# Optimization experiments

Hardware: AMD Instinct MI355X
Metric: run time of the kernel (lower is better)

## Reference

```python
import jax, jax.numpy as jnp
import numpy as np

B, T1, T2, NFEAT, H = 8, 512, 1500, 1024, 16
DK = NFEAT // H


def setup_inputs() -> dict:
    key = jax.random.key(0)
    ks = jax.random.split(key, 8)
    s = 0.02
    return {
        "x": jax.random.normal(ks[0], (B, T1, NFEAT), dtype=jnp.float32),
        "memory": jax.random.normal(ks[1], (B, T2, NFEAT), dtype=jnp.float32),
        "memory_mask": jnp.ones((B, 1, T2), dtype=jnp.int32),
        "Wq": jax.random.normal(ks[2], (NFEAT, NFEAT), dtype=jnp.float32) * s,
        "bq": jnp.zeros((NFEAT,), dtype=jnp.float32),
        "Wkv": jax.random.normal(ks[3], (NFEAT, 2 * NFEAT), dtype=jnp.float32) * s,
        "bkv": jnp.zeros((2 * NFEAT,), dtype=jnp.float32),
        "Wout": jax.random.normal(ks[4], (NFEAT, NFEAT), dtype=jnp.float32) * s,
        "bout": jnp.zeros((NFEAT,), dtype=jnp.float32),
    }


def reference(x, memory, memory_mask, Wq, bq, Wkv, bkv, Wout, bout):
    b, t1, _ = x.shape
    t2 = memory.shape[1]
    # projections (W stored as (in, out))
    q = x @ Wq + bq                                   # (b, t1, n_feat)
    kv = memory @ Wkv + bkv                           # (b, t2, 2*n_feat)
    k, v = jnp.split(kv, 2, axis=-1)
    q_h = q.reshape(b, t1, H, DK).transpose(0, 2, 1, 3)   # (b,h,t1,dk)
    k_h = k.reshape(b, t2, H, DK).transpose(0, 2, 1, 3)   # (b,h,t2,dk)
    v_h = v.reshape(b, t2, H, DK).transpose(0, 2, 1, 3)   # (b,h,t2,dk)
    q_h = q_h * (DK ** -0.5)
    scores = jnp.einsum("bhqd,bhkd->bhqk", q_h, k_h)      # (b,h,t1,t2)
    mask0 = (memory_mask[:, None, :, :] == 0)             # (b,1,1 or t1,t2)
    scores = jnp.where(mask0, -jnp.inf, scores)
    attn = jax.nn.softmax(scores, axis=-1)
    attn = jnp.where(mask0, 0.0, attn)
    ctx = jnp.einsum("bhqk,bhkd->bhqd", attn, v_h)        # (b,h,t1,dk)
    ctx = ctx.transpose(0, 2, 1, 3).reshape(b, t1, H * DK)
    return ctx @ Wout + bout
```

## Files before the change

kernel.cpp:

```cpp
#include <hip/hip_runtime.h>
#include <cstdint>
#include <cstddef>

typedef __attribute__((ext_vector_type(8))) short short8;
typedef __attribute__((ext_vector_type(4))) float f32x4;

typedef __attribute__((address_space(3))) unsigned int lds_u32;
typedef const __attribute__((address_space(1))) unsigned int glb_u32;

__device__ __forceinline__ void gl_lds16(const void* g, void* l) {
  __builtin_amdgcn_global_load_lds((glb_u32*)g, (lds_u32*)l, 16, 0, 0);
}

__device__ __forceinline__ unsigned short bf16_rne(float f) {
  unsigned int u = __float_as_uint(f);
  u += 0x7FFFu + ((u >> 16) & 1u);
  return (unsigned short)(u >> 16);
}

__global__ void __launch_bounds__(256) k_cvt(const float* __restrict__ in,
                                             unsigned short* __restrict__ out, int n8) {
  int i = blockIdx.x * 256 + threadIdx.x;
  if (i >= n8) return;
  float4 a = reinterpret_cast<const float4*>(in)[2 * i];
  float4 b = reinterpret_cast<const float4*>(in)[2 * i + 1];
  short8 v;
  v[0] = (short)bf16_rne(a.x); v[1] = (short)bf16_rne(a.y);
  v[2] = (short)bf16_rne(a.z); v[3] = (short)bf16_rne(a.w);
  v[4] = (short)bf16_rne(b.x); v[5] = (short)bf16_rne(b.y);
  v[6] = (short)bf16_rne(b.z); v[7] = (short)bf16_rne(b.w);
  reinterpret_cast<short8*>(out)[i] = v;
}

__global__ void __launch_bounds__(256) k_tcvt(const float* __restrict__ W,
                                              unsigned short* __restrict__ WT,
                                              int R, int C) {
  __shared__ float t[64][65];
  const int c0 = blockIdx.x * 64, r0 = blockIdx.y * 64;
  const int lr = threadIdx.x >> 6, lc = threadIdx.x & 63;
#pragma unroll
  for (int i = 0; i < 16; ++i)
    t[i * 4 + lr][lc] = W[(size_t)(r0 + i * 4 + lr) * C + c0 + lc];
  __syncthreads();
#pragma unroll
  for (int i = 0; i < 16; ++i) {
    int ro = i * 4 + lr;
    WT[(size_t)(c0 + ro) * R + r0 + lc] = bf16_rne(t[lc][ro]);
  }
}

__global__ void __launch_bounds__(256) k_pad(unsigned short* __restrict__ pk,
                                             unsigned short* __restrict__ pv) {
  int i = blockIdx.x * 256 + threadIdx.x;
  if (i >= 128 * 36 * 64) return;
  int head = i / (36 * 64);
  int rem = i - head * (36 * 64);
  int t2 = rem / 64 + 1500;
  int dk = rem & 63;
  size_t ik = ((size_t)(head * 24 + 23) * 8 + (dk >> 3)) * 512 + (t2 & 63) * 8 + (dk & 7);
  size_t iv = ((size_t)(head * 24 + 23) * 8 + ((t2 >> 3) & 7)) * 512 + dk * 8 + (t2 & 7);
  pk[ik] = 0;
  pv[iv] = 0;
}

template <int MODE>
__global__ void __launch_bounds__(256) k_gemm(const unsigned short* __restrict__ A,
                                              const unsigned short* __restrict__ BT,
                                              const float* __restrict__ bias,
                                              void* __restrict__ out1,
                                              void* __restrict__ out2,
                                              int M, int K) {
  __shared__ unsigned short As[128 * 64];
  __shared__ unsigned short Bs[128 * 64];
  const int tid = threadIdx.x;
  const int lane = tid & 63;
  const int wid = tid >> 6;
  const int grp = lane >> 4, lm = lane & 15;

  constexpr int NBY = (MODE == 1) ? 16 : 8;
  constexpr int NWG = (MODE == 1) ? 94 * 16 : 32 * 8;
  constexpr int CPX = NWG / 8;
  const int bid = blockIdx.x;
  const int logical = (bid & 7) * CPX + (bid >> 3);
  const int m0 = (logical / NBY) * 128, n0 = (logical % NBY) * 128;

  const int wm = (wid >> 1) * 64, wn = (wid & 1) * 64;
  const int srow = tid >> 3;
  const int sx = ((tid & 7) * 16) ^ ((srow & 7) << 4);

  f32x4 acc[4][4] = {};

  const int nkt = K >> 6;
  for (int kt = 0; kt < nkt; ++kt) {
    __syncthreads();
#pragma unroll
    for (int c = 0; c < 4; ++c) {
      int row = c * 32 + srow;
      int ra = m0 + row; if (ra > M - 1) ra = M - 1;
      gl_lds16(A + (size_t)ra * K + kt * 64 + (sx >> 1), As + c * 2048 + tid * 8);
      gl_lds16(BT + (size_t)(n0 + row) * K + kt * 64 + (sx >> 1), Bs + c * 2048 + tid * 8);
    }
    __syncthreads();

    short8 af[4][2], bfr[4][2];
#pragma unroll
    for (int m = 0; m < 4; ++m)
#pragma unroll
      for (int ks = 0; ks < 2; ++ks) {
        int row = wm + m * 16 + lm;
        int off = (ks * 64 + grp * 16) ^ ((row & 7) << 4);
        af[m][ks] = *reinterpret_cast<const short8*>(&As[row * 64 + (off >> 1)]);
      }
#pragma unroll
    for (int n = 0; n < 4; ++n)
#pragma unroll
      for (int ks = 0; ks < 2; ++ks) {
        int row = wn + n * 16 + lm;
        int off = (ks * 64 + grp * 16) ^ ((row & 7) << 4);
        bfr[n][ks] = *reinterpret_cast<const short8*>(&Bs[row * 64 + (off >> 1)]);
      }
#pragma unroll
    for (int m = 0; m < 4; ++m)
#pragma unroll
      for (int n = 0; n < 4; ++n)
#pragma unroll
        for (int ks = 0; ks < 2; ++ks)
          acc[m][n] = __builtin_amdgcn_mfma_f32_16x16x32_bf16(af[m][ks], bfr[n][ks],
                                                              acc[m][n], 0, 0, 0);
  }

#pragma unroll
  for (int m = 0; m < 4; ++m) {
    int rbase = m0 + wm + m * 16 + grp * 4;
#pragma unroll
    for (int n = 0; n < 4; ++n) {
      int cg = n0 + wn + n * 16 + lm;
      float bs = bias[cg];
#pragma unroll
      for (int r = 0; r < 4; ++r) {
        int row = rbase + r;
        float v = acc[m][n][r] + bs;
        if (MODE == 0) {
          v *= 0.180336884f;
          int b = row >> 9, t1 = row & 511, h = cg >> 6, dk = cg & 63;
          ((unsigned short*)out1)[(((size_t)b * 16 + h) * 512 + t1) * 64 + dk] = bf16_rne(v);
        } else if (MODE == 1) {
          if (row < M) {
            int b = row / 1500, t2 = row - b * 1500;
            if (cg < 1024) {
              int h = cg >> 6, dk = cg & 63;
              int head = b * 16 + h;
              size_t idx = ((size_t)(head * 24 + (t2 >> 6)) * 8 + (dk >> 3)) * 512 +
                           (t2 & 63) * 8 + (dk & 7);
              ((unsigned short*)out1)[idx] = bf16_rne(v);
            } else {
              int h = (cg - 1024) >> 6, dk = (cg - 1024) & 63;
              int head = b * 16 + h;
              size_t idx = ((size_t)(head * 24 + (t2 >> 6)) * 8 + ((t2 >> 3) & 7)) * 512 +
                           dk * 8 + (t2 & 7);
              ((unsigned short*)out2)[idx] = bf16_rne(v);
            }
          }
        } else {
          ((float*)out1)[(size_t)row * 1024 + cg] = v;
        }
      }
    }
  }
}

__global__ void __launch_bounds__(256) k_attn(const unsigned short* __restrict__ Q,
                                              const unsigned short* __restrict__ PK,
                                              const unsigned short* __restrict__ PV,
                                              const int* __restrict__ mask,
                                              float* __restrict__ po,
                                              float* __restrict__ dn) {
  __shared__ unsigned short Ps[4][16 * 64];
  const int tid = threadIdx.x, lane = tid & 63, wid = tid >> 6;
  const int grp = lane >> 4, lm = lane & 15;
  const int bid = blockIdx.x;
  const int logical = (bid & 7) * 256 + (bid >> 3);
  const int head = logical >> 4, qt = (logical >> 1) & 7, half = logical & 1;
  const int b = head >> 4, h = head & 15;
  const int kt0 = half * 12;

  const unsigned short* qbase = Q + ((size_t)head * 512 + qt * 64) * 64;
  const unsigned short* kf = PK + (size_t)head * 98304 + grp * 512 + lm * 8;
  const unsigned short* vf = PV + (size_t)head * 98304 + grp * 512 + lm * 8;
  const int* mrow = mask + b * 1500;

  short8 aq[2];
#pragma unroll
  for (int ks = 0; ks < 2; ++ks)
    aq[ks] = *reinterpret_cast<const short8*>(qbase + (wid * 16 + lm) * 64 + ks * 32 + grp * 8);

  unsigned long long mlo = 0ull;
#pragma unroll
  for (int i = 0; i < 48; ++i) {
    int col = (kt0 + (i >> 2)) * 64 + (i & 3) * 16 + lm;
    unsigned int ok = (col < 1500) ? (mrow[col] != 0 ? 1u : 0u) : 0u;
    mlo |= (unsigned long long)ok << i;
  }

  f32x4 O[4] = {};
  f32x4 O4 = {0.f, 0.f, 0.f, 0.f};
  const short8 onesb = {(short)0x3F80, (short)0x3F80, (short)0x3F80, (short)0x3F80,
                        (short)0x3F80, (short)0x3F80, (short)0x3F80, (short)0x3F80};

  short8 bk[4][2];
#pragma unroll
  for (int n = 0; n < 4; ++n)
#pragma unroll
    for (int ks = 0; ks < 2; ++ks)
      bk[n][ks] = *reinterpret_cast<const short8*>(kf + (size_t)kt0 * 4096 + ks * 2048 + n * 128);

  for (int kt = kt0; kt < kt0 + 12; ++kt) {
    short8 bv[4][2];
#pragma unroll
    for (int n2 = 0; n2 < 4; ++n2)
#pragma unroll
      for (int ks = 0; ks < 2; ++ks)
        bv[n2][ks] = *reinterpret_cast<const short8*>(vf + (size_t)kt * 4096 + ks * 2048 + n2 * 128);

    f32x4 s[4];
#pragma unroll
    for (int n = 0; n < 4; ++n) {
      s[n] = f32x4{0.f, 0.f, 0.f, 0.f};
#pragma unroll
      for (int ks = 0; ks < 2; ++ks)
        s[n] = __builtin_amdgcn_mfma_f32_16x16x32_bf16(aq[ks], bk[n][ks], s[n], 0, 0, 0);
    }

    if (kt < kt0 + 11) {
#pragma unroll
      for (int n = 0; n < 4; ++n)
#pragma unroll
        for (int ks = 0; ks < 2; ++ks)
          bk[n][ks] = *reinterpret_cast<const short8*>(
              kf + (size_t)(kt + 1) * 4096 + ks * 2048 + n * 128);
    }

    unsigned int nib = (unsigned int)mlo & 15u;
    mlo >>= 4;
    float mb4[4];
#pragma unroll
    for (int n = 0; n < 4; ++n) mb4[n] = (nib >> n) & 1u ? -8.0f : -3.0e38f;
#pragma unroll
    for (int n = 0; n < 4; ++n)
#pragma unroll
      for (int r = 0; r < 4; ++r) s[n][r] = exp2f(s[n][r] + mb4[n]);

#pragma unroll
    for (int n = 0; n < 4; ++n)
#pragma unroll
      for (int r = 0; r < 4; ++r) {
        int prow = grp * 4 + r;
        int pb = (n * 16 + lm) * 2;
        Ps[wid][prow * 64 + ((pb ^ ((prow & 7) << 4)) >> 1)] = bf16_rne(s[n][r]);
      }
    short8 pa[2];
#pragma unroll
    for (int ks = 0; ks < 2; ++ks) {
      int off = (ks * 64 + grp * 16) ^ ((lm & 7) << 4);
      pa[ks] = *reinterpret_cast<const short8*>(&Ps[wid][lm * 64 + (off >> 1)]);
    }

#pragma unroll
    for (int n2 = 0; n2 < 4; ++n2)
#pragma unroll
      for (int ks = 0; ks < 2; ++ks)
        O[n2] = __builtin_amdgcn_mfma_f32_16x16x32_bf16(pa[ks], bv[n2][ks], O[n2], 0, 0, 0);
#pragma unroll
    for (int ks = 0; ks < 2; ++ks)
      O4 = __builtin_amdgcn_mfma_f32_16x16x32_bf16(pa[ks], onesb, O4, 0, 0, 0);
  }

  float* orow = po + (size_t)half * 4194304 +
                ((size_t)(b * 512 + qt * 64 + wid * 16 + grp * 4)) * 1024 + h * 64;
#pragma unroll
  for (int r = 0; r < 4; ++r)
#pragma unroll
    for (int n2 = 0; n2 < 4; ++n2)
      orow[r * 1024 + n2 * 16 + lm] = O[n2][r];
  if (lm == 0) {
    int t1g = b * 512 + qt * 64 + wid * 16 + grp * 4;
#pragma unroll
    for (int r = 0; r < 4; ++r)
      dn[half * 65536 + (t1g + r) * 16 + h] = O4[r];
  }
}

__global__ void __launch_bounds__(256) k_comb(const float* __restrict__ po,
                                              const float* __restrict__ dn,
                                              unsigned short* __restrict__ ctx) {
  int idx = blockIdx.x * 256 + threadIdx.x;
  if (idx >= 524288) return;
  int row = idx >> 7, c8 = idx & 127;
  int col0 = c8 * 8, h = c8 >> 3;
  float d = dn[row * 16 + h] + dn[65536 + row * 16 + h];
  float inv = 1.0f / d;
  const float4* p0 = reinterpret_cast<const float4*>(po + (size_t)row * 1024 + col0);
  const float4* p1 = reinterpret_cast<const float4*>(po + 4194304 + (size_t)row * 1024 + col0);
  float4 a0 = p0[0], a1 = p0[1], b0 = p1[0], b1 = p1[1];
  short8 v;
  v[0] = (short)bf16_rne((a0.x + b0.x) * inv);
  v[1] = (short)bf16_rne((a0.y + b0.y) * inv);
  v[2] = (short)bf16_rne((a0.z + b0.z) * inv);
  v[3] = (short)bf16_rne((a0.w + b0.w) * inv);
  v[4] = (short)bf16_rne((a1.x + b1.x) * inv);
  v[5] = (short)bf16_rne((a1.y + b1.y) * inv);
  v[6] = (short)bf16_rne((a1.z + b1.z) * inv);
  v[7] = (short)bf16_rne((a1.w + b1.w) * inv);
  reinterpret_cast<short8*>(ctx)[idx] = v;
}

extern "C" void kernel_launch(void* const* d_in, const int* in_sizes, int n_in,
                              void* d_out, int out_size, void* d_ws, size_t ws_size,
                              hipStream_t stream) {
  const float* x = (const float*)d_in[0];
  const float* mem = (const float*)d_in[1];
  const int* mask = (const int*)d_in[2];
  const float* Wq = (const float*)d_in[3];
  const float* bq = (const float*)d_in[4];
  const float* Wkv = (const float*)d_in[5];
  const float* bkv = (const float*)d_in[6];
  const float* Wout = (const float*)d_in[7];
  const float* bout = (const float*)d_in[8];

  uint8_t* w = (uint8_t*)d_ws;
  unsigned short* xb    = (unsigned short*)(w);
  unsigned short* mb    = (unsigned short*)(w + 8388608);
  unsigned short* wqT   = (unsigned short*)(w + 32964608);
  unsigned short* wkvT  = (unsigned short*)(w + 35061760);
  unsigned short* woutT = (unsigned short*)(w + 39256064);
  unsigned short* qb    = (unsigned short*)(w + 41353216);
  unsigned short* kb    = (unsigned short*)(w + 49741824);
  unsigned short* vtb   = (unsigned short*)(w + 74907648);
  unsigned short* ctx   = (unsigned short*)(w + 100073472);
  float* po             = (float*)(w);
  float* dn             = (float*)(w + 33554432);

  k_cvt<<<2048, 256, 0, stream>>>(x, xb, 524288);
  k_cvt<<<6000, 256, 0, stream>>>(mem, mb, 1536000);
  k_tcvt<<<dim3(16, 16), 256, 0, stream>>>(Wq, wqT, 1024, 1024);
  k_tcvt<<<dim3(32, 16), 256, 0, stream>>>(Wkv, wkvT, 1024, 2048);
  k_tcvt<<<dim3(16, 16), 256, 0, stream>>>(Wout, woutT, 1024, 1024);
  k_pad<<<1152, 256, 0, stream>>>(kb, vtb);
  k_gemm<0><<<256, 256, 0, stream>>>(xb, wqT, bq, qb, nullptr, 4096, 1024);
  k_gemm<1><<<1504, 256, 0, stream>>>(mb, wkvT, bkv, kb, vtb, 12000, 1024);
  k_attn<<<2048, 256, 0, stream>>>(qb, kb, vtb, mask, po, dn);
  k_comb<<<2048, 256, 0, stream>>>(po, dn, ctx);
  k_gemm<2><<<256, 256, 0, stream>>>(ctx, woutT, bout, d_out, nullptr, 4096, 1024);
}
```

Before: 233.0 us.

## Double-buffer GEMM LDS tiles and merge prep kernels into one launch

The GEMM now keeps two LDS buffers, issuing the async global-to-LDS loads for the next K tile before running the MFMAs on the current one. This cuts the loop to one barrier per iteration and is meant to hide load latency. Separately, the six conversion, transpose and padding launches are fused into a single block-indexed k_prep kernel to save launch overhead. Doubling LDS to 64KB per block may lower occupancy.

```diff
diff --git a/kernel.cpp b/kernel.cpp
--- a/kernel.cpp
+++ b/kernel.cpp
@@ -18,9 +18,9 @@
   return (unsigned short)(u >> 16);
 }
 
-__global__ void __launch_bounds__(256) k_cvt(const float* __restrict__ in,
-                                             unsigned short* __restrict__ out, int n8) {
-  int i = blockIdx.x * 256 + threadIdx.x;
+__device__ __forceinline__ void cvt_body(const float* __restrict__ in,
+                                         unsigned short* __restrict__ out,
+                                         int i, int n8) {
   if (i >= n8) return;
   float4 a = reinterpret_cast<const float4*>(in)[2 * i];
   float4 b = reinterpret_cast<const float4*>(in)[2 * i + 1];
@@ -32,35 +32,52 @@
   reinterpret_cast<short8*>(out)[i] = v;
 }
 
-__global__ void __launch_bounds__(256) k_tcvt(const float* __restrict__ W,
-                                              unsigned short* __restrict__ WT,
-                                              int R, int C) {
+__global__ void __launch_bounds__(256) k_prep(const float* __restrict__ x,
+                                              const float* __restrict__ mem,
+                                              const float* __restrict__ Wq,
+                                              const float* __restrict__ Wkv,
+                                              const float* __restrict__ Wout,
+                                              unsigned short* __restrict__ xb,
+                                              unsigned short* __restrict__ mb,
+                                              unsigned short* __restrict__ wqT,
+                                              unsigned short* __restrict__ wkvT,
+                                              unsigned short* __restrict__ woutT,
+                                              unsigned short* __restrict__ pk,
+                                              unsigned short* __restrict__ pv) {
   __shared__ float t[64][65];
-  const int c0 = blockIdx.x * 64, r0 = blockIdx.y * 64;
-  const int lr = threadIdx.x >> 6, lc = threadIdx.x & 63;
-#pragma unroll
-  for (int i = 0; i < 16; ++i)
-    t[i * 4 + lr][lc] = W[(size_t)(r0 + i * 4 + lr) * C + c0 + lc];
-  __syncthreads();
-#pragma unroll
-  for (int i = 0; i < 16; ++i) {
-    int ro = i * 4 + lr;
-    WT[(size_t)(c0 + ro) * R + r0 + lc] = bf16_rne(t[lc][ro]);
-  }
-}
-
-__global__ void __launch_bounds__(256) k_pad(unsigned short* __restrict__ pk,
-                                             unsigned short* __restrict__ pv) {
-  int i = blockIdx.x * 256 + threadIdx.x;
-  if (i >= 128 * 36 * 64) return;
-  int head = i / (36 * 64);
-  int rem = i - head * (36 * 64);
-  int t2 = rem / 64 + 1500;
-  int dk = rem & 63;
-  size_t ik = ((size_t)(head * 24 + 23) * 8 + (dk >> 3)) * 512 + (t2 & 63) * 8 + (dk & 7);
-  size_t iv = ((size_t)(head * 24 + 23) * 8 + ((t2 >> 3) & 7)) * 512 + dk * 8 + (t2 & 7);
-  pk[ik] = 0;
-  pv[iv] = 0;
+  const int bid = blockIdx.x, tid = threadIdx.x;
+  if (bid < 2048) {
+    cvt_body(x, xb, bid * 256 + tid, 524288);
+  } else if (bid < 8048) {
+    cvt_body(mem, mb, (bid - 2048) * 256 + tid, 1536000);
+  } else if (bid < 9072) {
+    const float* W; unsigned short* WT; int R = 1024, C; int bid2, bx, by;
+    if (bid < 8304)      { W = Wq;   WT = wqT;   C = 1024; bid2 = bid - 8048; bx = bid2 & 15; by = bid2 >> 4; }
+    else if (bid < 8816) { W = Wkv;  WT = wkvT;  C = 2048; bid2 = bid - 8304; bx = bid2 & 31; by = bid2 >> 5; }
+    else                 { W = Wout; WT = woutT; C = 1024; bid2 = bid - 8816; bx = bid2 & 15; by = bid2 >> 4; }
+    const int c0 = bx * 64, r0 = by * 64;
+    const int lr = tid >> 6, lc = tid & 63;
+#pragma unroll
+    for (int i = 0; i < 16; ++i)
+      t[i * 4 + lr][lc] = W[(size_t)(r0 + i * 4 + lr) * C + c0 + lc];
+    __syncthreads();
+#pragma unroll
+    for (int i = 0; i < 16; ++i) {
+      int ro = i * 4 + lr;
+      WT[(size_t)(c0 + ro) * R + r0 + lc] = bf16_rne(t[lc][ro]);
+    }
+  } else {
+    int i = (bid - 9072) * 256 + tid;
+    if (i >= 128 * 36 * 64) return;
+    int head = i / (36 * 64);
+    int rem = i - head * (36 * 64);
+    int t2 = rem / 64 + 1500;
+    int dk = rem & 63;
+    size_t ik = ((size_t)(head * 24 + 23) * 8 + (dk >> 3)) * 512 + (t2 & 63) * 8 + (dk & 7);
+    size_t iv = ((size_t)(head * 24 + 23) * 8 + ((t2 >> 3) & 7)) * 512 + dk * 8 + (t2 & 7);
+    pk[ik] = 0;
+    pv[iv] = 0;
+  }
 }
 
 template <int MODE>
@@ -70,8 +87,8 @@
                                               void* __restrict__ out1,
                                               void* __restrict__ out2,
                                               int M, int K) {
-  __shared__ unsigned short As[128 * 64];
-  __shared__ unsigned short Bs[128 * 64];
+  __shared__ unsigned short As[2][128 * 64];
+  __shared__ unsigned short Bs[2][128 * 64];
   const int tid = threadIdx.x;
   const int lane = tid & 63;
   const int wid = tid >> 6;
@@ -88,20 +105,33 @@
   const int srow = tid >> 3;
   const int sx = ((tid & 7) * 16) ^ ((srow & 7) << 4);
 
+  const int nkt = K >> 6;
+#pragma unroll
+  for (int c = 0; c < 4; ++c) {
+    int row = c * 32 + srow;
+    int ra = m0 + row; if (ra > M - 1) ra = M - 1;
+    gl_lds16(A + (size_t)ra * K + (sx >> 1), &As[0][c * 2048 + tid * 8]);
+    gl_lds16(BT + (size_t)(n0 + row) * K + (sx >> 1), &Bs[0][c * 2048 + tid * 8]);
+  }
+  __syncthreads();
+
   f32x4 acc[4][4] = {};
-
-  const int nkt = K >> 6;
+  int cur = 0;
   for (int kt = 0; kt < nkt; ++kt) {
-    __syncthreads();
-#pragma unroll
-    for (int c = 0; c < 4; ++c) {
-      int row = c * 32 + srow;
-      int ra = m0 + row; if (ra > M - 1) ra = M - 1;
-      gl_lds16(A + (size_t)ra * K + kt * 64 + (sx >> 1), As + c * 2048 + tid * 8);
-      gl_lds16(BT + (size_t)(n0 + row) * K + kt * 64 + (sx >> 1), Bs + c * 2048 + tid * 8);
-    }
-    __syncthreads();
-
+    if (kt + 1 < nkt) {
+#pragma unroll
+      for (int c = 0; c < 4; ++c) {
+        int row = c * 32 + srow;
+        int ra = m0 + row; if (ra > M - 1) ra = M - 1;
+        gl_lds16(A + (size_t)ra * K + (kt + 1) * 64 + (sx >> 1),
+                 &As[cur ^ 1][c * 2048 + tid * 8]);
+        gl_lds16(BT + (size_t)(n0 + row) * K + (kt + 1) * 64 + (sx >> 1),
+                 &Bs[cur ^ 1][c * 2048 + tid * 8]);
+      }
+    }
+
+    const unsigned short* Ab = &As[cur][0];
+    const unsigned short* Bb = &Bs[cur][0];
     short8 af[4][2], bfr[4][2];
 #pragma unroll
     for (int m = 0; m < 4; ++m)
@@ -109,7 +139,7 @@
       for (int ks = 0; ks < 2; ++ks) {
         int row = wm + m * 16 + lm;
         int off = (ks * 64 + grp * 16) ^ ((row & 7) << 4);
-        af[m][ks] = *reinterpret_cast<const short8*>(&As[row * 64 + (off >> 1)]);
+        af[m][ks] = *reinterpret_cast<const short8*>(&Ab[row * 64 + (off >> 1)]);
       }
 #pragma unroll
     for (int n = 0; n < 4; ++n)
@@ -117,7 +147,7 @@
       for (int ks = 0; ks < 2; ++ks) {
         int row = wn + n * 16 + lm;
         int off = (ks * 64 + grp * 16) ^ ((row & 7) << 4);
-        bfr[n][ks] = *reinterpret_cast<const short8*>(&Bs[row * 64 + (off >> 1)]);
+        bfr[n][ks] = *reinterpret_cast<const short8*>(&Bb[row * 64 + (off >> 1)]);
       }
 #pragma unroll
     for (int m = 0; m < 4; ++m)
@@ -127,6 +157,8 @@
         for (int ks = 0; ks < 2; ++ks)
           acc[m][n] = __builtin_amdgcn_mfma_f32_16x16x32_bf16(af[m][ks], bfr[n][ks],
                                                               acc[m][n], 0, 0, 0);
+    __syncthreads();
+    cur ^= 1;
   }
 
 #pragma unroll
@@ -340,12 +372,7 @@
   float* po             = (float*)(w);
   float* dn             = (float*)(w + 33554432);
 
-  k_cvt<<<2048, 256, 0, stream>>>(x, xb, 524288);
-  k_cvt<<<6000, 256, 0, stream>>>(mem, mb, 1536000);
-  k_tcvt<<<dim3(16, 16), 256, 0, stream>>>(Wq, wqT, 1024, 1024);
-  k_tcvt<<<dim3(32, 16), 256, 0, stream>>>(Wkv, wkvT, 1024, 2048);
-  k_tcvt<<<dim3(16, 16), 256, 0, stream>>>(Wout, woutT, 1024, 1024);
-  k_pad<<<1152, 256, 0, stream>>>(kb, vtb);
+  k_prep<<<10224, 256, 0, stream>>>(x, mem, Wq, Wkv, Wout, xb, mb, wqT, wkvT, woutT, kb, vtb);
   k_gemm<0><<<256, 256, 0, stream>>>(xb, wqT, bq, qb, nullptr, 4096, 1024);
   k_gemm<1><<<1504, 256, 0, stream>>>(mb, wkvT, bkv, kb, vtb, 12000, 1024);
   k_attn<<<2048, 256, 0, stream>>>(qb, kb, vtb, mask, po, dn);
```

Result: faster. 219.1 us (-5.9%).

## Pre-swizzle operands into MFMA fragment layout, drop LDS staging, fuse combine into out-proj

Applied to the files above, without the earlier changes.

All bf16 conversions, weight transposes and K/V padding now run in one prep kernel, which writes A and B operands in a fragment-major layout. The GEMM loads its MFMA fragments straight from global memory into registers with a two-stage register double buffer, replacing LDS staging and block barriers. The split-softmax combine kernel is removed: the output projection GEMM reads the two partial fp32 accumulators and denominators, normalises them and converts to bf16 inline. This cuts launches and intermediate traffic, but each wave now re-reads operands from global or L2 with no LDS sharing, and the out-proj reads fp32 data redundantly across N blocks.

```diff
diff --git a/kernel.cpp b/kernel.cpp
--- a/kernel.cpp
+++ b/kernel.cpp
@@ -4,13 +4,6 @@
 
 typedef __attribute__((ext_vector_type(8))) short short8;
 typedef __attribute__((ext_vector_type(4))) float f32x4;
-
-typedef __attribute__((address_space(3))) unsigned int lds_u32;
-typedef const __attribute__((address_space(1))) unsigned int glb_u32;
-
-__device__ __forceinline__ void gl_lds16(const void* g, void* l) {
-  __builtin_amdgcn_global_load_lds((glb_u32*)g, (lds_u32*)l, 16, 0, 0);
-}
 
 __device__ __forceinline__ unsigned short bf16_rne(float f) {
   unsigned int u = __float_as_uint(f);
@@ -18,116 +11,161 @@
   return (unsigned short)(u >> 16);
 }
 
-__global__ void __launch_bounds__(256) k_cvt(const float* __restrict__ in,
-                                             unsigned short* __restrict__ out, int n8) {
-  int i = blockIdx.x * 256 + threadIdx.x;
-  if (i >= n8) return;
-  float4 a = reinterpret_cast<const float4*>(in)[2 * i];
-  float4 b = reinterpret_cast<const float4*>(in)[2 * i + 1];
-  short8 v;
-  v[0] = (short)bf16_rne(a.x); v[1] = (short)bf16_rne(a.y);
-  v[2] = (short)bf16_rne(a.z); v[3] = (short)bf16_rne(a.w);
-  v[4] = (short)bf16_rne(b.x); v[5] = (short)bf16_rne(b.y);
-  v[6] = (short)bf16_rne(b.z); v[7] = (short)bf16_rne(b.w);
-  reinterpret_cast<short8*>(out)[i] = v;
-}
-
-__global__ void __launch_bounds__(256) k_tcvt(const float* __restrict__ W,
-                                              unsigned short* __restrict__ WT,
-                                              int R, int C) {
-  __shared__ float t[64][65];
-  const int c0 = blockIdx.x * 64, r0 = blockIdx.y * 64;
-  const int lr = threadIdx.x >> 6, lc = threadIdx.x & 63;
-#pragma unroll
-  for (int i = 0; i < 16; ++i)
-    t[i * 4 + lr][lc] = W[(size_t)(r0 + i * 4 + lr) * C + c0 + lc];
-  __syncthreads();
-#pragma unroll
-  for (int i = 0; i < 16; ++i) {
-    int ro = i * 4 + lr;
-    WT[(size_t)(c0 + ro) * R + r0 + lc] = bf16_rne(t[lc][ro]);
-  }
-}
-
-__global__ void __launch_bounds__(256) k_pad(unsigned short* __restrict__ pk,
-                                             unsigned short* __restrict__ pv) {
-  int i = blockIdx.x * 256 + threadIdx.x;
-  if (i >= 128 * 36 * 64) return;
-  int head = i / (36 * 64);
-  int rem = i - head * (36 * 64);
-  int t2 = rem / 64 + 1500;
-  int dk = rem & 63;
-  size_t ik = ((size_t)(head * 24 + 23) * 8 + (dk >> 3)) * 512 + (t2 & 63) * 8 + (dk & 7);
-  size_t iv = ((size_t)(head * 24 + 23) * 8 + ((t2 >> 3) & 7)) * 512 + dk * 8 + (t2 & 7);
-  pk[ik] = 0;
-  pv[iv] = 0;
+__device__ __forceinline__ short8 pack8(const float* v) {
+  short8 r;
+#pragma unroll
+  for (int e = 0; e < 8; ++e) r[e] = (short)bf16_rne(v[e]);
+  return r;
+}
+
+__global__ void __launch_bounds__(256) k_prep(const float* __restrict__ x,
+                                              const float* __restrict__ mem,
+                                              const float* __restrict__ Wq,
+                                              const float* __restrict__ Wkv,
+                                              const float* __restrict__ Wout,
+                                              unsigned short* __restrict__ xp,
+                                              unsigned short* __restrict__ mp,
+                                              unsigned short* __restrict__ wqp,
+                                              unsigned short* __restrict__ wkvp,
+                                              unsigned short* __restrict__ wop,
+                                              unsigned short* __restrict__ pk,
+                                              unsigned short* __restrict__ pv) {
+  const int bid = blockIdx.x, tid = threadIdx.x;
+  if (bid < 8048) {
+    const float* in; unsigned short* out; int s;
+    if (bid < 2048) { in = x;   out = xp; s = bid * 256 + tid; }
+    else            { in = mem; out = mp; s = (bid - 2048) * 256 + tid; }
+    int row = s >> 7, col8 = s & 127;
+    int grp = col8 & 3, ks = (col8 >> 2) & 1, kt = col8 >> 3;
+    float4 a = *reinterpret_cast<const float4*>(in + (size_t)row * 1024 + col8 * 8);
+    float4 b = *reinterpret_cast<const float4*>(in + (size_t)row * 1024 + col8 * 8 + 4);
+    float v[8] = {a.x, a.y, a.z, a.w, b.x, b.y, b.z, b.w};
+    int mblk = row >> 7, rloc = row & 127;
+    size_t d = ((((size_t)(mblk * 16 + kt) * 2 + ks) * 4 + grp) * 128 + rloc) * 8;
+    *reinterpret_cast<short8*>(out + d) = pack8(v);
+  } else if (bid < 8064) {
+    int p = (bid - 8048) * 256 + tid;
+    if (p >= 4096) return;
+    int rloc = 96 + (p >> 7), col8 = p & 127;
+    int grp = col8 & 3, ks = (col8 >> 2) & 1, kt = col8 >> 3;
+    size_t d = ((((size_t)(93 * 16 + kt) * 2 + ks) * 4 + grp) * 128 + rloc) * 8;
+    short8 z = {};
+    *reinterpret_cast<short8*>(mp + d) = z;
+  } else if (bid < 10112) {
+    const float* W; unsigned short* out; int C, w0;
+    if (bid < 8576)      { W = Wq;   out = wqp;  C = 1024; w0 = (bid - 8064) * 256 + tid; }
+    else if (bid < 9600) { W = Wkv;  out = wkvp; C = 2048; w0 = (bid - 8576) * 256 + tid; }
+    else                 { W = Wout; out = wop;  C = 1024; w0 = (bid - 9600) * 256 + tid; }
+    int rowN = w0 & 127; int t = w0 >> 7;
+    int grp = t & 3; t >>= 2;
+    int ks = t & 1; t >>= 1;
+    int kt = t & 15; int nblk = t >> 4;
+    int n = nblk * 128 + rowN;
+    int k0 = kt * 64 + ks * 32 + grp * 8;
+    float v[8];
+#pragma unroll
+    for (int e = 0; e < 8; ++e) v[e] = W[(size_t)(k0 + e) * C + n];
+    *reinterpret_cast<short8*>(out + (size_t)w0 * 8) = pack8(v);
+  } else {
+    int i = (bid - 10112) * 256 + tid;
+    if (i >= 128 * 36 * 64) return;
+    int head = i / (36 * 64);
+    int rem = i - head * (36 * 64);
+    int t2 = rem / 64 + 1500;
+    int dk = rem & 63;
+    size_t ik = ((size_t)(head * 24 + 23) * 8 + (dk >> 3)) * 512 + (t2 & 63) * 8 + (dk & 7);
+    size_t iv = ((size_t)(head * 24 + 23) * 8 + ((t2 >> 3) & 7)) * 512 + dk * 8 + (t2 & 7);
+    pk[ik] = 0;
+    pv[iv] = 0;
+  }
 }
 
 template <int MODE>
-__global__ void __launch_bounds__(256) k_gemm(const unsigned short* __restrict__ A,
-                                              const unsigned short* __restrict__ BT,
+__global__ void __launch_bounds__(256) k_gemm(const unsigned short* __restrict__ Ap,
+                                              const unsigned short* __restrict__ Bp,
                                               const float* __restrict__ bias,
                                               void* __restrict__ out1,
                                               void* __restrict__ out2,
-                                              int M, int K) {
-  __shared__ unsigned short As[128 * 64];
-  __shared__ unsigned short Bs[128 * 64];
-  const int tid = threadIdx.x;
-  const int lane = tid & 63;
-  const int wid = tid >> 6;
+                                              const float* __restrict__ po,
+                                              const float* __restrict__ dn,
+                                              int M) {
+  const int tid = threadIdx.x, lane = tid & 63, wid = tid >> 6;
   const int grp = lane >> 4, lm = lane & 15;
-
   constexpr int NBY = (MODE == 1) ? 16 : 8;
   constexpr int NWG = (MODE == 1) ? 94 * 16 : 32 * 8;
   constexpr int CPX = NWG / 8;
+  constexpr int NKT = 16;
   const int bid = blockIdx.x;
   const int logical = (bid & 7) * CPX + (bid >> 3);
-  const int m0 = (logical / NBY) * 128, n0 = (logical % NBY) * 128;
-
+  const int mblk = logical / NBY, nblk = logical % NBY;
+  const int m0 = mblk * 128, n0 = nblk * 128;
   const int wm = (wid >> 1) * 64, wn = (wid & 1) * 64;
-  const int srow = tid >> 3;
-  const int sx = ((tid & 7) * 16) ^ ((srow & 7) << 4);
+
+  const unsigned short* ab = Ap + (size_t)mblk * 131072 + grp * 1024 + (wm + lm) * 8;
+  const unsigned short* bb = Bp + (size_t)nblk * 131072 + grp * 1024 + (wn + lm) * 8;
 
   f32x4 acc[4][4] = {};
-
-  const int nkt = K >> 6;
-  for (int kt = 0; kt < nkt; ++kt) {
-    __syncthreads();
-#pragma unroll
-    for (int c = 0; c < 4; ++c) {
-      int row = c * 32 + srow;
-      int ra = m0 + row; if (ra > M - 1) ra = M - 1;
-      gl_lds16(A + (size_t)ra * K + kt * 64 + (sx >> 1), As + c * 2048 + tid * 8);
-      gl_lds16(BT + (size_t)(n0 + row) * K + kt * 64 + (sx >> 1), Bs + c * 2048 + tid * 8);
-    }
-    __syncthreads();
-
-    short8 af[4][2], bfr[4][2];
-#pragma unroll
-    for (int m = 0; m < 4; ++m)
-#pragma unroll
-      for (int ks = 0; ks < 2; ++ks) {
-        int row = wm + m * 16 + lm;
-        int off = (ks * 64 + grp * 16) ^ ((row & 7) << 4);
-        af[m][ks] = *reinterpret_cast<const short8*>(&As[row * 64 + (off >> 1)]);
-      }
-#pragma unroll
-    for (int n = 0; n < 4; ++n)
-#pragma unroll
-      for (int ks = 0; ks < 2; ++ks) {
-        int row = wn + n * 16 + lm;
-        int off = (ks * 64 + grp * 16) ^ ((row & 7) << 4);
-        bfr[n][ks] = *reinterpret_cast<const short8*>(&Bs[row * 64 + (off >> 1)]);
-      }
-#pragma unroll
-    for (int m = 0; m < 4; ++m)
-#pragma unroll
-      for (int n = 0; n < 4; ++n)
-#pragma unroll
-        for (int ks = 0; ks < 2; ++ks)
-          acc[m][n] = __builtin_amdgcn_mfma_f32_16x16x32_bf16(af[m][ks], bfr[n][ks],
-                                                              acc[m][n], 0, 0, 0);
-  }
+  short8 aA[4][2], bA[4][2], aB[4][2], bB[4][2];
+
+#define LOADB_(dst, kt)                                                          \
+  {                                                                              \
+    _Pragma("unroll") for (int n = 0; n < 4; ++n)                                \
+        _Pragma("unroll") for (int ks = 0; ks < 2; ++ks)                         \
+            dst[n][ks] = *reinterpret_cast<const short8*>(                       \
+                bb + ((kt) * 2 + ks) * 4096 + n * 128);                          \
+  }
+#define LOADA_(dst, kt)                                                          \
+  {                                                                              \
+    if (MODE != 2) {                                                             \
+      _Pragma("unroll") for (int m = 0; m < 4; ++m)                              \
+          _Pragma("unroll") for (int ks = 0; ks < 2; ++ks)                       \
+              dst[m][ks] = *reinterpret_cast<const short8*>(                     \
+                  ab + ((kt) * 2 + ks) * 4096 + m * 128);                        \
+    } else {                                                                     \
+      _Pragma("unroll") for (int m = 0; m < 4; ++m) {                            \
+        int row = m0 + wm + m * 16 + lm;             \
+        float inv = 1.0f / (dn[row * 16 + (kt)] + dn[65536 + row * 16 + (kt)]);  \
+        _Pragma("unroll") for (int ks = 0; ks < 2; ++ks) {                       \
+          const float* p0 = po + (size_t)row * 1024 + (kt) * 64 + ks * 32 + grp * 8; \
+          const float* p1 = p0 + 4194304;                                        \
+          float4 x0 = *reinterpret_cast<const float4*>(p0);                      \
+          float4 x1 = *reinterpret_cast<const float4*>(p0 + 4);                  \
+          float4 y0 = *reinterpret_cast<const float4*>(p1);                      \
+          float4 y1 = *reinterpret_cast<const float4*>(p1 + 4);                  \
+          float v[8] = {(x0.x + y0.x) * inv, (x0.y + y0.y) * inv,                \
+                        (x0.z + y0.z) * inv, (x0.w + y0.w) * inv,                \
+                        (x1.x + y1.x) * inv, (x1.y + y1.y) * inv,                \
+                        (x1.z + y1.z) * inv, (x1.w + y1.w) * inv};               \
+          dst[m][ks] = pack8(v);                                                 \
+        }                                                                        \
+      }                                                                          \
+    }                                                                            \
+  }
+#define MFMA_(a, b)                                                              \
+  {                                                                              \
+    _Pragma("unroll") for (int m = 0; m < 4; ++m)                                \
+        _Pragma("unroll") for (int n = 0; n < 4; ++n)                            \
+            _Pragma("unroll") for (int ks = 0; ks < 2; ++ks)                     \
+                acc[m][n] = __builtin_amdgcn_mfma_f32_16x16x32_bf16(             \
+                    a[m][ks], b[n][ks], acc[m][n], 0, 0, 0);                     \
+  }
+
+  LOADA_(aA, 0);
+  LOADB_(bA, 0);
+  for (int kt2 = 0; kt2 < NKT / 2; ++kt2) {
+    const int ktb = 2 * kt2 + 1;
+    LOADA_(aB, ktb);
+    LOADB_(bB, ktb);
+    MFMA_(aA, bA);
+    if (ktb + 1 < NKT) {
+      LOADA_(aA, ktb + 1);
+      LOADB_(bA, ktb + 1);
+    }
+    MFMA_(aB, bB);
+  }
+#undef LOADA_
+#undef LOADB_
+#undef MFMA_
 
 #pragma unroll
   for (int m = 0; m < 4; ++m) {
@@ -290,30 +328,6 @@
   }
 }
 
-__global__ void __launch_bounds__(256) k_comb(const float* __restrict__ po,
-                                              const float* __restrict__ dn,
-                                              unsigned short* __restrict__ ctx) {
-  int idx = blockIdx.x * 256 + threadIdx.x;
-  if (idx >= 524288) return;
-  int row = idx >> 7, c8 = idx & 127;
-  int col0 = c8 * 8, h = c8 >> 3;
-  float d = dn[row * 16 + h] + dn[65536 + row * 16 + h];
-  float inv = 1.0f / d;
-  const float4* p0 = reinterpret_cast<const float4*>(po + (size_t)row * 1024 + col0);
-  const float4* p1 = reinterpret_cast<const float4*>(po + 4194304 + (size_t)row * 1024 + col0);
-  float4 a0 = p0[0], a1 = p0[1], b0 = p1[0], b1 = p1[1];
-  short8 v;
-  v[0] = (short)bf16_rne((a0.x + b0.x) * inv);
-  v[1] = (short)bf16_rne((a0.y + b0.y) * inv);
-  v[2] = (short)bf16_rne((a0.z + b0.z) * inv);
-  v[3] = (short)bf16_rne((a0.w + b0.w) * inv);
-  v[4] = (short)bf16_rne((a1.x + b1.x) * inv);
-  v[5] = (short)bf16_rne((a1.y + b1.y) * inv);
-  v[6] = (short)bf16_rne((a1.z + b1.z) * inv);
-  v[7] = (short)bf16_rne((a1.w + b1.w) * inv);
-  reinterpret_cast<short8*>(ctx)[idx] = v;
-}
-
 extern "C" void kernel_launch(void* const* d_in, const int* in_sizes, int n_in,
                               void* d_out, int out_size, void* d_ws, size_t ws_size,
                               hipStream_t stream) {
@@ -328,27 +342,20 @@
   const float* bout = (const float*)d_in[8];
 
   uint8_t* w = (uint8_t*)d_ws;
-  unsigned short* xb    = (unsigned short*)(w);
-  unsigned short* mb    = (unsigned short*)(w + 8388608);
-  unsigned short* wqT   = (unsigned short*)(w + 32964608);
-  unsigned short* wkvT  = (unsigned short*)(w + 35061760);
-  unsigned short* woutT = (unsigned short*)(w + 39256064);
-  unsigned short* qb    = (unsigned short*)(w + 41353216);
-  unsigned short* kb    = (unsigned short*)(w + 49741824);
-  unsigned short* vtb   = (unsigned short*)(w + 74907648);
-  unsigned short* ctx   = (unsigned short*)(w + 100073472);
-  float* po             = (float*)(w);
-  float* dn             = (float*)(w + 33554432);
-
-  k_cvt<<<2048, 256, 0, stream>>>(x, xb, 524288);
-  k_cvt<<<6000, 256, 0, stream>>>(mem, mb, 1536000);
-  k_tcvt<<<dim3(16, 16), 256, 0, stream>>>(Wq, wqT, 1024, 1024);
-  k_tcvt<<<dim3(32, 16), 256, 0, stream>>>(Wkv, wkvT, 1024, 2048);
-  k_tcvt<<<dim3(16, 16), 256, 0, stream>>>(Wout, woutT, 1024, 1024);
-  k_pad<<<1152, 256, 0, stream>>>(kb, vtb);
-  k_gemm<0><<<256, 256, 0, stream>>>(xb, wqT, bq, qb, nullptr, 4096, 1024);
-  k_gemm<1><<<1504, 256, 0, stream>>>(mb, wkvT, bkv, kb, vtb, 12000, 1024);
+  unsigned short* xbp  = (unsigned short*)(w);
+  unsigned short* mbp  = (unsigned short*)(w + 8388608);
+  unsigned short* wqp  = (unsigned short*)(w + 33030144);
+  unsigned short* wkvp = (unsigned short*)(w + 35127296);
+  unsigned short* wop  = (unsigned short*)(w + 39321600);
+  unsigned short* qb   = (unsigned short*)(w + 41418752);
+  unsigned short* kb   = (unsigned short*)(w + 49807360);
+  unsigned short* vtb  = (unsigned short*)(w + 74973184);
+  float* po            = (float*)(w);
+  float* dn            = (float*)(w + 35127296);
+
+  k_prep<<<11264, 256, 0, stream>>>(x, mem, Wq, Wkv, Wout, xbp, mbp, wqp, wkvp, wop, kb, vtb);
+  k_gemm<0><<<256, 256, 0, stream>>>(xbp, wqp, bq, qb, nullptr, nullptr, nullptr, 4096);
+  k_gemm<1><<<1504, 256, 0, stream>>>(mbp, wkvp, bkv, kb, vtb, nullptr, nullptr, 12000);
   k_attn<<<2048, 256, 0, stream>>>(qb, kb, vtb, mask, po, dn);
-  k_comb<<<2048, 256, 0, stream>>>(po, dn, ctx);
-  k_gemm<2><<<256, 256, 0, stream>>>(ctx, woutT, bout, d_out, nullptr, 4096, 1024);
-}
+  k_gemm<2><<<256, 256, 0, stream>>>(nullptr, wop, bout, d_out, nullptr, po, dn, 4096);
+}
```

Measured after the change: 274.6 us. +17.9%, slower.
